# Optimization experiments

Measured on AMD Instinct MI355X. Metric: run time of the kernel, lower is better.

Reference implementation:

```python
import jax, jax.numpy as jnp
import numpy as np

B, U, V = 4, 64, 256
IN_DIM, STATE_DIM, CODE_DIM = 768, 768, 384
NUM_HEADS, HEAD_DIM = 8, 64
INNER = NUM_HEADS * HEAD_DIM  # 512
SCALE = HEAD_DIM ** 0.5


def _ln(x, g, b, eps=1e-5):
    mu = jnp.mean(x, axis=-1, keepdims=True)
    var = jnp.var(x, axis=-1, keepdims=True)
    return (x - mu) * jax.lax.rsqrt(var + eps) * g + b


def setup_inputs() -> dict:
    key = jax.random.key(0)
    ks = jax.random.split(key, 12)
    def w(k, shape, s=0.02):
        return jax.random.normal(k, shape, jnp.float32) * s
    return {
        "receiver_states": jax.random.normal(ks[0], (B, U, STATE_DIM), jnp.float32),
        "receiver_codes": jax.random.normal(ks[1], (B, U, CODE_DIM), jnp.float32),
        "sender_states": jax.random.normal(ks[2], (B, V, IN_DIM), jnp.float32),
        "ln_r_g": jnp.ones((STATE_DIM,), jnp.float32),
        "ln_r_b": jnp.zeros((STATE_DIM,), jnp.float32),
        "ln_s_g": jnp.ones((IN_DIM,), jnp.float32),
        "ln_s_b": jnp.zeros((IN_DIM,), jnp.float32),
        "Wq": w(ks[3], (STATE_DIM, INNER)), "bq": jnp.zeros((INNER,), jnp.float32), "Wmq": w(ks[4], (CODE_DIM, STATE_DIM)),
        "Wk": w(ks[5], (IN_DIM, INNER)),   "bk": jnp.zeros((INNER,), jnp.float32), "Wmk": w(ks[6], (CODE_DIM, IN_DIM)),
        "Wv": w(ks[7], (IN_DIM, INNER)),   "bv": jnp.zeros((INNER,), jnp.float32), "Wmv": w(ks[8], (CODE_DIM, IN_DIM)),
        "We": w(ks[9], (INNER, STATE_DIM)), "be": jnp.zeros((STATE_DIM,), jnp.float32), "Wme": w(ks[10], (CODE_DIM, INNER)),
        "gamma": jnp.ones((STATE_DIM,), jnp.float32),  # LayerScale, init 1.0
    }


def reference(receiver_states, receiver_codes, sender_states,
              ln_r_g, ln_r_b, ln_s_g, ln_s_b,
              Wq, bq, Wmq, Wk, bk, Wmk, Wv, bv, Wmv, We, be, Wme, gamma):
    r = _ln(receiver_states, ln_r_g, ln_r_b)   # (b,u,ds)
    s = _ln(sender_states, ln_s_g, ln_s_b)     # (b,v,di)
    # ModFC: y = (x * (1 + ctx @ Wm)) @ W + b  (code-conditioned input modulation)
    q = (r * (1.0 + receiver_codes @ Wmq)) @ Wq + bq          # (b,u,inner)
    mk = 1.0 + receiver_codes @ Wmk                           # (b,u,di)
    mv = 1.0 + receiver_codes @ Wmv                           # (b,u,di)
    xs = s[:, :, None, :]                                     # (b,v,1,di)
    k = (xs * mk[:, None, :, :]) @ Wk + bk                    # (b,v,u,inner)
    v = (xs * mv[:, None, :, :]) @ Wv + bv                    # (b,v,u,inner)
    qh = q.reshape(B, U, NUM_HEADS, HEAD_DIM)
    kh = k.reshape(B, V, U, NUM_HEADS, HEAD_DIM)
    vh = v.reshape(B, V, U, NUM_HEADS, HEAD_DIM)
    scores = jnp.einsum('buhc,bvuhc->bhuv', qh, kh) / SCALE   # (b,h,u,v)
    weights = jax.nn.softmax(scores, axis=-1)
    msg = jnp.einsum('bhuv,bvuhc->buhc', weights, vh).reshape(B, U, INNER)
    out = (msg * (1.0 + receiver_codes @ Wme)) @ We + be      # exit ModFC -> (b,u,ds)
    out = out * gamma                                         # LayerScale
    return receiver_states + out                              # residual
```

## Files before the change

### kernel.cpp

```cpp
#include <hip/hip_runtime.h>


#define DD 768
#define CDIM 384
#define NH 8
#define HD 64
#define INNER 512
#define VV 256

__device__ __forceinline__ void fma4(float4& a, float s, const float4& b) {
  a.x += s * b.x; a.y += s * b.y; a.z += s * b.z; a.w += s * b.w;
}

template <int K, int NS>
__device__ __forceinline__ void gcore(const float* __restrict__ A0, int lda,
                                      const float* __restrict__ Bp,
                                      float4& a0, float4& a1, float4& a2,
                                      float4& a3) {
  float4 b0[8], b1[8];
#pragma unroll
  for (int i = 0; i < 8; i++) b0[i] = *(const float4*)(Bp + (size_t)i * NS);
  const float* Bq = Bp + (size_t)8 * NS;
#pragma unroll 1
  for (int kk = 0; kk < K; kk += 16) {
#pragma unroll
    for (int i = 0; i < 8; i++) b1[i] = *(const float4*)(Bq + (size_t)i * NS);
    Bq += (size_t)8 * NS;
#pragma unroll
    for (int c = 0; c < 2; c++) {
      int kb = kk + c * 4;
      float4 f0 = *(const float4*)(A0 + kb);
      float4 f1 = *(const float4*)(A0 + lda + kb);
      float4 f2 = *(const float4*)(A0 + 2 * lda + kb);
      float4 f3 = *(const float4*)(A0 + 3 * lda + kb);
      float4 bv;
      bv = b0[c*4+0]; fma4(a0,f0.x,bv); fma4(a1,f1.x,bv); fma4(a2,f2.x,bv); fma4(a3,f3.x,bv);
      bv = b0[c*4+1]; fma4(a0,f0.y,bv); fma4(a1,f1.y,bv); fma4(a2,f2.y,bv); fma4(a3,f3.y,bv);
      bv = b0[c*4+2]; fma4(a0,f0.z,bv); fma4(a1,f1.z,bv); fma4(a2,f2.z,bv); fma4(a3,f3.z,bv);
      bv = b0[c*4+3]; fma4(a0,f0.w,bv); fma4(a1,f1.w,bv); fma4(a2,f2.w,bv); fma4(a3,f3.w,bv);
    }
    if (kk + 16 < K) {
#pragma unroll
      for (int i = 0; i < 8; i++) b0[i] = *(const float4*)(Bq + (size_t)i * NS);
      Bq += (size_t)8 * NS;
    }
#pragma unroll
    for (int c = 0; c < 2; c++) {
      int kb = kk + 8 + c * 4;
      float4 f0 = *(const float4*)(A0 + kb);
      float4 f1 = *(const float4*)(A0 + lda + kb);
      float4 f2 = *(const float4*)(A0 + 2 * lda + kb);
      float4 f3 = *(const float4*)(A0 + 3 * lda + kb);
      float4 bv;
      bv = b1[c*4+0]; fma4(a0,f0.x,bv); fma4(a1,f1.x,bv); fma4(a2,f2.x,bv); fma4(a3,f3.x,bv);
      bv = b1[c*4+1]; fma4(a0,f0.y,bv); fma4(a1,f1.y,bv); fma4(a2,f2.y,bv); fma4(a3,f3.y,bv);
      bv = b1[c*4+2]; fma4(a0,f0.z,bv); fma4(a1,f1.z,bv); fma4(a2,f2.z,bv); fma4(a3,f3.z,bv);
      bv = b1[c*4+3]; fma4(a0,f0.w,bv); fma4(a1,f1.w,bv); fma4(a2,f2.w,bv); fma4(a3,f3.w,bv);
    }
  }
}

__global__ __launch_bounds__(256, 2) void k_s1(
    const float* __restrict__ ss, const float* __restrict__ rs,
    const float* __restrict__ g_s, const float* __restrict__ b_s,
    const float* __restrict__ g_r, const float* __restrict__ b_r,
    const float* __restrict__ codes, const float* __restrict__ Wmq,
    const float* __restrict__ Wmk, const float* __restrict__ Wmv,
    const float* __restrict__ Wme, const float* __restrict__ Wk,
    const float* __restrict__ be, const float* __restrict__ gamma,
    float* __restrict__ s_ln, float* __restrict__ r_ln,
    float* __restrict__ cp, float* __restrict__ WkT,
    float* __restrict__ outp) {
  __shared__ __align__(16) float SB[6400];
  int bid = blockIdx.x, t = threadIdx.x;
  if (bid < 176) {
    int nc = bid % 11, mb = bid / 11;
    int base = nc * 256;
    const float* W; int N, colW;
    if (base < 768)       { W = Wmq; N = DD;    colW = base; }
    else if (base < 1536) { W = Wmk; N = DD;    colW = base - 768; }
    else if (base < 2304) { W = Wmv; N = DD;    colW = base - 1536; }
    else                  { W = Wme; N = INNER; colW = base - 2304; }
    int m0 = mb * 16;
#pragma unroll
    for (int p = 0; p < 24; p++) {
      int idx = p * 256 + t, r = idx / 384, k = idx % 384;
      SB[idx] = codes[(size_t)(m0 + r) * CDIM + k];
    }
    __syncthreads();
    int kl = t & 63, wid = t >> 6;
    const float* A0 = SB + (wid * 4) * 384;
    float4 a0 = {0,0,0,0}, a1 = {0,0,0,0}, a2 = {0,0,0,0}, a3 = {0,0,0,0};
    if (N == DD)
      gcore<384, DD>(A0, 384, W + colW + 4 * kl, a0, a1, a2, a3);
    else
      gcore<384, INNER>(A0, 384, W + colW + 4 * kl, a0, a1, a2, a3);
    int m = m0 + wid * 4, gcol = base + 4 * kl;
    *(float4*)(cp + (size_t)m * 2816 + gcol) = a0;
    *(float4*)(cp + (size_t)(m + 1) * 2816 + gcol) = a1;
    *(float4*)(cp + (size_t)(m + 2) * 2816 + gcol) = a2;
    *(float4*)(cp + (size_t)(m + 3) * 2816 + gcol) = a3;
  } else if (bid < 272) {
    int tid = bid - 176;
    int d0 = (tid >> 3) * 64, c0 = (tid & 7) * 64;
    int j = t & 63, i0 = t >> 6;
#pragma unroll
    for (int p = 0; p < 16; p++) {
      int i = p * 4 + i0;
      SB[i * 65 + j] = Wk[(size_t)(d0 + i) * INNER + c0 + j];
    }
    __syncthreads();
#pragma unroll
    for (int p = 0; p < 16; p++) {
      int i = p * 4 + i0;
      WkT[(size_t)(c0 + i) * DD + d0 + j] = SB[j * 65 + i];
    }
  } else {
    int rr = bid - 272;
    const float *x, *g, *bb; float* y; int r; bool isR;
    if (rr < 1024) { x = ss; g = g_s; bb = b_s; y = s_ln; r = rr; isR = false; }
    else           { x = rs; g = g_r; bb = b_r; y = r_ln; r = rr - 1024; isR = true; }
    const float* xr = x + (size_t)r * DD;
    float v0 = xr[t], v1 = xr[t + 256], v2 = xr[t + 512];
    float s = v0 + v1 + v2, sq = v0 * v0 + v1 * v1 + v2 * v2;
    for (int o = 32; o > 0; o >>= 1) {
      s += __shfl_down(s, o, 64); sq += __shfl_down(sq, o, 64);
    }
    int wid = t >> 6, lane = t & 63;
    if (lane == 0) { SB[wid] = s; SB[wid + 4] = sq; }
    __syncthreads();
    float sum = SB[0] + SB[1] + SB[2] + SB[3];
    float ssq = SB[4] + SB[5] + SB[6] + SB[7];
    float mu = sum * (1.0f / 768.0f);
    float var = ssq * (1.0f / 768.0f) - mu * mu;
    float rstd = rsqrtf(var + 1e-5f);
    float* yr = y + (size_t)r * DD;
    yr[t]       = (v0 - mu) * rstd * g[t]       + bb[t];
    yr[t + 256] = (v1 - mu) * rstd * g[t + 256] + bb[t + 256];
    yr[t + 512] = (v2 - mu) * rstd * g[t + 512] + bb[t + 512];
    if (isR) {
      float* orow = outp + (size_t)r * DD;
      orow[t]       = v0 + be[t]       * gamma[t];
      orow[t + 256] = v1 + be[t + 256] * gamma[t + 256];
      orow[t + 512] = v2 + be[t + 512] * gamma[t + 512];
    }
  }
}

__global__ __launch_bounds__(256, 2) void k_s2(
    const float* __restrict__ s_ln, const float* __restrict__ r_ln,
    const float* __restrict__ cp, const float* __restrict__ Wq,
    float* __restrict__ sT, float* __restrict__ qp) {
  __shared__ __align__(16) float SB[4160];
  int bid = blockIdx.x, t = threadIdx.x;
  if (bid < 128) {
    int ks = bid & 3, t2 = bid >> 2, nc = t2 & 1, mb = t2 >> 1;
    int m0 = mb * 16, col0 = nc * 256, k0 = ks * 192;
#pragma unroll
    for (int p = 0; p < 12; p++) {
      int idx = p * 256 + t, r = idx / 192, k = idx % 192;
      int d = k0 + k;
      float mqv = cp[(size_t)(m0 + r) * 2816 + d] + 1.0f;
      SB[idx] = r_ln[(size_t)(m0 + r) * DD + d] * mqv;
    }
    __syncthreads();
    int kl = t & 63, wid = t >> 6;
    int col = col0 + 4 * kl;
    const float* A0 = SB + (wid * 4) * 192;
    float4 a0 = {0,0,0,0}, a1 = {0,0,0,0}, a2 = {0,0,0,0}, a3 = {0,0,0,0};
    gcore<192, INNER>(A0, 192, Wq + (size_t)k0 * INNER + col, a0, a1, a2, a3);
    int m = m0 + wid * 4;
    float* dst = qp + (size_t)ks * (256 * INNER);
    *(float4*)(dst + (size_t)m * INNER + col) = a0;
    *(float4*)(dst + (size_t)(m + 1) * INNER + col) = a1;
    *(float4*)(dst + (size_t)(m + 2) * INNER + col) = a2;
    *(float4*)(dst + (size_t)(m + 3) * INNER + col) = a3;
  } else {
    int tid = bid - 128;
    int vt = tid & 3, dt = (tid >> 2) % 12, b = tid / 48;
    int v0 = vt * 64, d0 = dt * 64;
    int j = t & 63, i0 = t >> 6;
#pragma unroll
    for (int p = 0; p < 16; p++) {
      int i = p * 4 + i0;
      SB[i * 65 + j] = s_ln[(size_t)(b * VV + v0 + i) * DD + d0 + j];
    }
    __syncthreads();
#pragma unroll
    for (int p = 0; p < 16; p++) {
      int i = p * 4 + i0;
      sT[((size_t)b * DD + d0 + i) * VV + v0 + j] = SB[j * 65 + i];
    }
  }
}

__global__ __launch_bounds__(256, 2) void k_s3(
    const float* __restrict__ qp, const float* __restrict__ bq,
    const float* __restrict__ WkT, const float* __restrict__ cp,
    const float* __restrict__ bk, float* __restrict__ qm,
    float* __restrict__ qbk) {
  __shared__ __align__(16) float SB[1024];
  int bid = blockIdx.x, t = threadIdx.x;
  if (bid < 384) {
    int h = bid & 7, dc = (bid >> 3) % 3, mb = bid / 24;
    int m0 = mb * 16;
#pragma unroll
    for (int p = 0; p < 4; p++) {
      int idx = p * 256 + t, r = idx >> 6, c = idx & 63;
      int i = h * HD + c;
      size_t off = (size_t)(m0 + r) * INNER + i;
      SB[idx] = qp[off] + qp[131072 + off] + qp[262144 + off] +
                qp[393216 + off] + bq[i];
    }
    __syncthreads();
    int kl = t & 63, wid = t >> 6;
    int col = dc * 256 + 4 * kl;
    const float* A0 = SB + (wid * 4) * HD;
    float4 a0 = {0,0,0,0}, a1 = {0,0,0,0}, a2 = {0,0,0,0}, a3 = {0,0,0,0};
    gcore<64, DD>(A0, HD, WkT + (size_t)(h * HD) * DD + col, a0, a1, a2, a3);
#pragma unroll
    for (int j = 0; j < 4; j++) {
      float4 a = (j == 0) ? a0 : (j == 1) ? a1 : (j == 2) ? a2 : a3;
      int m = m0 + wid * 4 + j;
      const float* mkp = cp + (size_t)m * 2816 + 768 + col;
      float4 o = {a.x * (mkp[0] + 1.0f), a.y * (mkp[1] + 1.0f),
                  a.z * (mkp[2] + 1.0f), a.w * (mkp[3] + 1.0f)};
      *(float4*)(qm + ((size_t)m * NH + h) * DD + col) = o;
    }
  } else {
    int m = bid - 384;
    size_t off = (size_t)m * INNER;
    SB[t] = (qp[off + t] + qp[131072 + off + t] + qp[262144 + off + t] +
             qp[393216 + off + t] + bq[t]) * bk[t];
    int t2 = t + 256;
    SB[t2] = (qp[off + t2] + qp[131072 + off + t2] + qp[262144 + off + t2] +
              qp[393216 + off + t2] + bq[t2]) * bk[t2];
    __syncthreads();
    if (t < 8) {
      float a = 0.f;
      for (int c = 0; c < HD; c++) a += SB[t * HD + c];
      qbk[m * NH + t] = a;
    }
  }
}

__global__ __launch_bounds__(256, 2) void k_s4(
    const float* __restrict__ qm, const float* __restrict__ sT,
    float* __restrict__ scp) {
  __shared__ __align__(16) float SB[3072];
  int bid = blockIdx.x, t = threadIdx.x;
  int ks = bid & 3, b = (bid >> 2) & 3, mb = bid >> 4;
  int gi0 = b * 512 + mb * 16, k0 = ks * 192;
#pragma unroll
  for (int p = 0; p < 12; p++) {
    int idx = p * 256 + t, r = idx / 192, k = idx % 192;
    SB[idx] = qm[(size_t)(gi0 + r) * DD + k0 + k];
  }
  __syncthreads();
  int kl = t & 63, wid = t >> 6;
  int col = 4 * kl;
  const float* A0 = SB + (wid * 4) * 192;
  float4 a0 = {0,0,0,0}, a1 = {0,0,0,0}, a2 = {0,0,0,0}, a3 = {0,0,0,0};
  gcore<192, VV>(A0, 192, sT + ((size_t)b * DD + k0) * VV + col, a0, a1, a2, a3);
  int gi = gi0 + wid * 4;
  float* dst = scp + (size_t)ks * (2048 * VV);
  *(float4*)(dst + (size_t)gi * VV + col) = a0;
  *(float4*)(dst + (size_t)(gi + 1) * VV + col) = a1;
  *(float4*)(dst + (size_t)(gi + 2) * VV + col) = a2;
  *(float4*)(dst + (size_t)(gi + 3) * VV + col) = a3;
}

__global__ __launch_bounds__(256, 2) void k_s5(
    const float* __restrict__ scp, const float* __restrict__ qbk,
    const float* __restrict__ s_ln, const float* __restrict__ cp,
    float* __restrict__ wsm) {
  __shared__ __align__(16) float SB[4096];
  int bid = blockIdx.x, t = threadIdx.x;
  int dc = bid % 3, up = (bid / 3) % 32, b = bid / 96;
  int gi0 = b * 512 + up * 16;
#pragma unroll
  for (int p = 0; p < 16; p++) {
    int idx = p * 256 + t, r = idx >> 8, c = idx & 255;
    size_t o = (size_t)(gi0 + r) * VV + c;
    float v = scp[o] + scp[524288 + o] + scp[1048576 + o] + scp[1572864 + o];
    int m = b * 64 + up * 2 + (r >> 3), h = r & 7;
    SB[idx] = (v + qbk[m * NH + h]) * 0.125f;
  }
  __syncthreads();
  int wid = t >> 6, lane = t & 63;
#pragma unroll
  for (int j = 0; j < 4; j++) {
    int r = wid * 4 + j;
    float x0 = SB[r * 256 + lane],       x1 = SB[r * 256 + lane + 64];
    float x2 = SB[r * 256 + lane + 128], x3 = SB[r * 256 + lane + 192];
    float mx = fmaxf(fmaxf(x0, x1), fmaxf(x2, x3));
    for (int o = 1; o < 64; o <<= 1) mx = fmaxf(mx, __shfl_xor(mx, o, 64));
    float e0 = __expf(x0 - mx), e1 = __expf(x1 - mx);
    float e2 = __expf(x2 - mx), e3 = __expf(x3 - mx);
    float sm = e0 + e1 + e2 + e3;
    for (int o = 1; o < 64; o <<= 1) sm += __shfl_xor(sm, o, 64);
    float rinv = 1.0f / sm;
    SB[r * 256 + lane] = e0 * rinv;       SB[r * 256 + lane + 64] = e1 * rinv;
    SB[r * 256 + lane + 128] = e2 * rinv; SB[r * 256 + lane + 192] = e3 * rinv;
  }
  __syncthreads();
  int kl = t & 63;
  int col = dc * 256 + 4 * kl;
  const float* A0 = SB + (wid * 4) * 256;
  float4 a0 = {0,0,0,0}, a1 = {0,0,0,0}, a2 = {0,0,0,0}, a3 = {0,0,0,0};
  gcore<VV, DD>(A0, 256, s_ln + (size_t)(b * VV) * DD + col, a0, a1, a2, a3);
#pragma unroll
  for (int j = 0; j < 4; j++) {
    float4 a = (j == 0) ? a0 : (j == 1) ? a1 : (j == 2) ? a2 : a3;
    int r = wid * 4 + j;
    int ul = r >> 3, h = r & 7, m = b * 64 + up * 2 + ul;
    const float* mvp = cp + (size_t)m * 2816 + 1536 + col;
    float4 o = {a.x * (mvp[0] + 1.0f), a.y * (mvp[1] + 1.0f),
                a.z * (mvp[2] + 1.0f), a.w * (mvp[3] + 1.0f)};
    *(float4*)(wsm + ((size_t)h * 256 + m) * DD + col) = o;
  }
}

__global__ __launch_bounds__(256, 2) void k_s6(
    const float* __restrict__ wsm, const float* __restrict__ Wv,
    float* __restrict__ mmp) {
  __shared__ __align__(16) float SB[6400];
  int bid = blockIdx.x, t = threadIdx.x;
  int hp = bid & 1, ks = (bid >> 1) & 7, mb = bid >> 4;
  int h0 = hp * 4, m0 = mb * 16, k0 = ks * 96;
#pragma unroll
  for (int p = 0; p < 24; p++) {
    int idx = p * 256 + t;
    int e = idx / 1536, rem = idx % 1536, r = rem / 96, k = rem % 96;
    SB[e * 1540 + r * 96 + k] =
        wsm[((size_t)(h0 + e) * 256 + m0 + r) * DD + k0 + k];
  }
  __syncthreads();
  int kl = t & 63, wid = t >> 6;
  int hs = kl >> 4, c4 = 4 * (kl & 15);
  int colg = h0 * HD + hs * HD + c4;
  const float* A0 = SB + hs * 1540 + (wid * 4) * 96;
  float4 a0 = {0,0,0,0}, a1 = {0,0,0,0}, a2 = {0,0,0,0}, a3 = {0,0,0,0};
  gcore<96, INNER>(A0, 96, Wv + (size_t)k0 * INNER + colg, a0, a1, a2, a3);
  float* dst = mmp + (size_t)ks * (256 * INNER);
  int m = m0 + wid * 4;
  *(float4*)(dst + (size_t)m * INNER + colg) = a0;
  *(float4*)(dst + (size_t)(m + 1) * INNER + colg) = a1;
  *(float4*)(dst + (size_t)(m + 2) * INNER + colg) = a2;
  *(float4*)(dst + (size_t)(m + 3) * INNER + colg) = a3;
}

__global__ __launch_bounds__(256, 2) void k_s7(
    const float* __restrict__ mmp, const float* __restrict__ bvv,
    const float* __restrict__ cp, const float* __restrict__ We,
    const float* __restrict__ gamma, float* __restrict__ outp) {
  __shared__ __align__(16) float SB[1024];
  int bid = blockIdx.x, t = threadIdx.x;
  int ks = bid & 7, dc = (bid >> 3) % 3, mb = bid / 24;
  int m0 = mb * 16, k0 = ks * 64;
#pragma unroll
  for (int p = 0; p < 4; p++) {
    int idx = p * 256 + t, r = idx >> 6, k = idx & 63;
    int i = k0 + k;
    size_t off = (size_t)(m0 + r) * INNER + i;
    float v = mmp[off] + mmp[131072 + off] + mmp[262144 + off] +
              mmp[393216 + off] + mmp[524288 + off] + mmp[655360 + off] +
              mmp[786432 + off] + mmp[917504 + off];
    float mev = cp[(size_t)(m0 + r) * 2816 + 2304 + i] + 1.0f;
    SB[idx] = (v + bvv[i]) * mev;
  }
  __syncthreads();
  int kl = t & 63, wid = t >> 6;
  int col = dc * 256 + 4 * kl;
  const float* A0 = SB + (wid * 4) * 64;
  float4 a0 = {0,0,0,0}, a1 = {0,0,0,0}, a2 = {0,0,0,0}, a3 = {0,0,0,0};
  gcore<64, DD>(A0, 64, We + (size_t)k0 * DD + col, a0, a1, a2, a3);
  float4 g4 = *(const float4*)(gamma + col);
  int m = m0 + wid * 4;
#pragma unroll
  for (int j = 0; j < 4; j++) {
    float4 a = (j == 0) ? a0 : (j == 1) ? a1 : (j == 2) ? a2 : a3;
    float* orow = outp + (size_t)(m + j) * DD + col;
    unsafeAtomicAdd(orow + 0, a.x * g4.x);
    unsafeAtomicAdd(orow + 1, a.y * g4.y);
    unsafeAtomicAdd(orow + 2, a.z * g4.z);
    unsafeAtomicAdd(orow + 3, a.w * g4.w);
  }
}

extern "C" void kernel_launch(void* const* d_in, const int* in_sizes, int n_in,
                              void* d_out, int out_size, void* d_ws, size_t ws_size,
                              hipStream_t stream) {
  const float* rs     = (const float*)d_in[0];
  const float* codes  = (const float*)d_in[1];
  const float* ss     = (const float*)d_in[2];
  const float* ln_r_g = (const float*)d_in[3];
  const float* ln_r_b = (const float*)d_in[4];
  const float* ln_s_g = (const float*)d_in[5];
  const float* ln_s_b = (const float*)d_in[6];
  const float* Wq  = (const float*)d_in[7];
  const float* bq  = (const float*)d_in[8];
  const float* Wmq = (const float*)d_in[9];
  const float* Wk  = (const float*)d_in[10];
  const float* bk  = (const float*)d_in[11];
  const float* Wmk = (const float*)d_in[12];
  const float* Wv  = (const float*)d_in[13];
  const float* bv  = (const float*)d_in[14];
  const float* Wmv = (const float*)d_in[15];
  const float* We  = (const float*)d_in[16];
  const float* be  = (const float*)d_in[17];
  const float* Wme = (const float*)d_in[18];
  const float* gamma = (const float*)d_in[19];

  float* w = (float*)d_ws;
  float* s_ln = w;
  float* r_ln = w + 786432;
  float* WkT  = w + 983040;
  float* qp   = w + 1376256;
  float* sT   = w + 1900544;
  float* cp   = w + 2686976;
  float* qbk  = w + 3407872;
  float* qm   = w + 3409920;
  float* scp  = w + 4982784;
  float* wsm  = qm;
  float* mmp  = r_ln;

  k_s1<<<dim3(1552), 256, 0, stream>>>(ss, rs, ln_s_g, ln_s_b, ln_r_g, ln_r_b,
                                       codes, Wmq, Wmk, Wmv, Wme, Wk, be, gamma,
                                       s_ln, r_ln, cp, WkT, (float*)d_out);
  k_s2<<<dim3(320), 256, 0, stream>>>(s_ln, r_ln, cp, Wq, sT, qp);
  k_s3<<<dim3(640), 256, 0, stream>>>(qp, bq, WkT, cp, bk, qm, qbk);
  k_s4<<<dim3(512), 256, 0, stream>>>(qm, sT, scp);
  k_s5<<<dim3(384), 256, 0, stream>>>(scp, qbk, s_ln, cp, wsm);
  k_s6<<<dim3(256), 256, 0, stream>>>(wsm, Wv, mmp);
  k_s7<<<dim3(384), 256, 0, stream>>>(mmp, bv, cp, We, gamma, (float*)d_out);
}
```

Baseline: 213.3 us.

## Convert weights to bf16 in a prepass and replace output atomics with split-K reduction kernel

A new prepass kernel converts all eight weight matrices to bf16 each call, writing Wk transposed, and every GEMM core now reads bf16 weights and expands them to fp32 in registers. The goal is to halve weight memory traffic in the FMA-based GEMMs. Separately, the exit projection now writes per-split partial sums to a workspace, and a new final kernel reduces them and applies residual, bias and gamma, replacing float atomics. In exchange it adds two launches and a full conversion pass every call, and bf16 weights reduce accuracy.

```diff
diff --git a/kernel.cpp b/kernel.cpp
--- a/kernel.cpp
+++ b/kernel.cpp
@@ -8,8 +8,23 @@
 #define INNER 512
 #define VV 256
 
+typedef unsigned short u16;
+
 __device__ __forceinline__ void fma4(float4& a, float s, const float4& b) {
   a.x += s * b.x; a.y += s * b.y; a.z += s * b.z; a.w += s * b.w;
+}
+
+__device__ __forceinline__ float4 bexp(uint2 u) {
+  float4 r;
+  r.x = __uint_as_float(u.x << 16);
+  r.y = __uint_as_float(u.x & 0xffff0000u);
+  r.z = __uint_as_float(u.y << 16);
+  r.w = __uint_as_float(u.y & 0xffff0000u);
+  return r;
+}
+
+__device__ __forceinline__ u16 f2b(float v) {
+  return (u16)((__float_as_uint(v) + 0x8000u) >> 16);
 }
 
 template <int K, int NS>
@@ -60,27 +75,113 @@
   }
 }
 
+template <int K, int NS>
+__device__ __forceinline__ void gcoreb(const float* __restrict__ A0, int lda,
+                                       const u16* __restrict__ Bp,
+                                       float4& a0, float4& a1, float4& a2,
+                                       float4& a3) {
+  uint2 b0[8], b1[8];
+#pragma unroll
+  for (int i = 0; i < 8; i++) b0[i] = *(const uint2*)(Bp + (size_t)i * NS);
+  const u16* Bq = Bp + (size_t)8 * NS;
+#pragma unroll 1
+  for (int kk = 0; kk < K; kk += 16) {
+#pragma unroll
+    for (int i = 0; i < 8; i++) b1[i] = *(const uint2*)(Bq + (size_t)i * NS);
+    Bq += (size_t)8 * NS;
+#pragma unroll
+    for (int c = 0; c < 2; c++) {
+      int kb = kk + c * 4;
+      float4 f0 = *(const float4*)(A0 + kb);
+      float4 f1 = *(const float4*)(A0 + lda + kb);
+      float4 f2 = *(const float4*)(A0 + 2 * lda + kb);
+      float4 f3 = *(const float4*)(A0 + 3 * lda + kb);
+      float4 bv;
+      bv = bexp(b0[c*4+0]); fma4(a0,f0.x,bv); fma4(a1,f1.x,bv); fma4(a2,f2.x,bv); fma4(a3,f3.x,bv);
+      bv = bexp(b0[c*4+1]); fma4(a0,f0.y,bv); fma4(a1,f1.y,bv); fma4(a2,f2.y,bv); fma4(a3,f3.y,bv);
+      bv = bexp(b0[c*4+2]); fma4(a0,f0.z,bv); fma4(a1,f1.z,bv); fma4(a2,f2.z,bv); fma4(a3,f3.z,bv);
+      bv = bexp(b0[c*4+3]); fma4(a0,f0.w,bv); fma4(a1,f1.w,bv); fma4(a2,f2.w,bv); fma4(a3,f3.w,bv);
+    }
+    if (kk + 16 < K) {
+#pragma unroll
+      for (int i = 0; i < 8; i++) b0[i] = *(const uint2*)(Bq + (size_t)i * NS);
+      Bq += (size_t)8 * NS;
+    }
+#pragma unroll
+    for (int c = 0; c < 2; c++) {
+      int kb = kk + 8 + c * 4;
+      float4 f0 = *(const float4*)(A0 + kb);
+      float4 f1 = *(const float4*)(A0 + lda + kb);
+      float4 f2 = *(const float4*)(A0 + 2 * lda + kb);
+      float4 f3 = *(const float4*)(A0 + 3 * lda + kb);
+      float4 bv;
+      bv = bexp(b1[c*4+0]); fma4(a0,f0.x,bv); fma4(a1,f1.x,bv); fma4(a2,f2.x,bv); fma4(a3,f3.x,bv);
+      bv = bexp(b1[c*4+1]); fma4(a0,f0.y,bv); fma4(a1,f1.y,bv); fma4(a2,f2.y,bv); fma4(a3,f3.y,bv);
+      bv = bexp(b1[c*4+2]); fma4(a0,f0.z,bv); fma4(a1,f1.z,bv); fma4(a2,f2.z,bv); fma4(a3,f3.z,bv);
+      bv = bexp(b1[c*4+3]); fma4(a0,f0.w,bv); fma4(a1,f1.w,bv); fma4(a2,f2.w,bv); fma4(a3,f3.w,bv);
+    }
+  }
+}
+
+
+__global__ __launch_bounds__(256) void k_s0(
+    const float* __restrict__ Wmq, const float* __restrict__ Wmk,
+    const float* __restrict__ Wmv, const float* __restrict__ Wme,
+    const float* __restrict__ Wq, const float* __restrict__ Wk,
+    const float* __restrict__ Wv, const float* __restrict__ We,
+    u16* __restrict__ bw) {
+  __shared__ float TL[64 * 65];
+  int bid = blockIdx.x, t = threadIdx.x;
+  if (bid < 96) {
+    int d0 = (bid >> 3) * 64, c0 = (bid & 7) * 64;
+    int j = t & 63, i0 = t >> 6;
+#pragma unroll
+    for (int p = 0; p < 16; p++) {
+      int i = p * 4 + i0;
+      TL[i * 65 + j] = Wk[(size_t)(d0 + i) * INNER + c0 + j];
+    }
+    __syncthreads();
+    u16* dst = bw + 2260992;
+#pragma unroll
+    for (int p = 0; p < 16; p++) {
+      int i = p * 4 + i0;
+      dst[(size_t)(c0 + i) * DD + d0 + j] = f2b(TL[j * 65 + i]);
+    }
+  } else {
+    for (int idx = (bid - 96) * 256 + t; idx < 565248; idx += 1184 * 256) {
+      const float* src; u16* dst; int off;
+      if (idx < 73728)       { src = Wmq; dst = bw;           off = idx; }
+      else if (idx < 147456) { src = Wmk; dst = bw + 294912;  off = idx - 73728; }
+      else if (idx < 221184) { src = Wmv; dst = bw + 589824;  off = idx - 147456; }
+      else if (idx < 270336) { src = Wme; dst = bw + 884736;  off = idx - 221184; }
+      else if (idx < 368640) { src = Wq;  dst = bw + 1081344; off = idx - 270336; }
+      else if (idx < 466944) { src = Wv;  dst = bw + 1474560; off = idx - 368640; }
+      else                   { src = We;  dst = bw + 1867776; off = idx - 466944; }
+      float4 v = *(const float4*)(src + (size_t)off * 4);
+      ushort4 o;
+      o.x = f2b(v.x); o.y = f2b(v.y); o.z = f2b(v.z); o.w = f2b(v.w);
+      *(ushort4*)(dst + (size_t)off * 4) = o;
+    }
+  }
+}
+
 __global__ __launch_bounds__(256, 2) void k_s1(
     const float* __restrict__ ss, const float* __restrict__ rs,
     const float* __restrict__ g_s, const float* __restrict__ b_s,
     const float* __restrict__ g_r, const float* __restrict__ b_r,
-    const float* __restrict__ codes, const float* __restrict__ Wmq,
-    const float* __restrict__ Wmk, const float* __restrict__ Wmv,
-    const float* __restrict__ Wme, const float* __restrict__ Wk,
-    const float* __restrict__ be, const float* __restrict__ gamma,
+    const float* __restrict__ codes, const u16* __restrict__ bw,
     float* __restrict__ s_ln, float* __restrict__ r_ln,
-    float* __restrict__ cp, float* __restrict__ WkT,
-    float* __restrict__ outp) {
+    float* __restrict__ cp) {
   __shared__ __align__(16) float SB[6400];
   int bid = blockIdx.x, t = threadIdx.x;
   if (bid < 176) {
     int nc = bid % 11, mb = bid / 11;
     int base = nc * 256;
-    const float* W; int N, colW;
-    if (base < 768)       { W = Wmq; N = DD;    colW = base; }
-    else if (base < 1536) { W = Wmk; N = DD;    colW = base - 768; }
-    else if (base < 2304) { W = Wmv; N = DD;    colW = base - 1536; }
-    else                  { W = Wme; N = INNER; colW = base - 2304; }
+    const u16* W; int N, colW;
+    if (base < 768)       { W = bw;          N = DD;    colW = base; }
+    else if (base < 1536) { W = bw + 294912; N = DD;    colW = base - 768; }
+    else if (base < 2304) { W = bw + 589824; N = DD;    colW = base - 1536; }
+    else                  { W = bw + 884736; N = INNER; colW = base - 2304; }
     int m0 = mb * 16;
 #pragma unroll
     for (int p = 0; p < 24; p++) {
@@ -92,34 +193,19 @@
     const float* A0 = SB + (wid * 4) * 384;
     float4 a0 = {0,0,0,0}, a1 = {0,0,0,0}, a2 = {0,0,0,0}, a3 = {0,0,0,0};
     if (N == DD)
-      gcore<384, DD>(A0, 384, W + colW + 4 * kl, a0, a1, a2, a3);
+      gcoreb<384, DD>(A0, 384, W + colW + 4 * kl, a0, a1, a2, a3);
     else
-      gcore<384, INNER>(A0, 384, W + colW + 4 * kl, a0, a1, a2, a3);
+      gcoreb<384, INNER>(A0, 384, W + colW + 4 * kl, a0, a1, a2, a3);
     int m = m0 + wid * 4, gcol = base + 4 * kl;
     *(float4*)(cp + (size_t)m * 2816 + gcol) = a0;
     *(float4*)(cp + (size_t)(m + 1) * 2816 + gcol) = a1;
     *(float4*)(cp + (size_t)(m + 2) * 2816 + gcol) = a2;
     *(float4*)(cp + (size_t)(m + 3) * 2816 + gcol) = a3;
-  } else if (bid < 272) {
-    int tid = bid - 176;
-    int d0 = (tid >> 3) * 64, c0 = (tid & 7) * 64;
-    int j = t & 63, i0 = t >> 6;
-#pragma unroll
-    for (int p = 0; p < 16; p++) {
-      int i = p * 4 + i0;
-      SB[i * 65 + j] = Wk[(size_t)(d0 + i) * INNER + c0 + j];
-    }
-    __syncthreads();
-#pragma unroll
-    for (int p = 0; p < 16; p++) {
-      int i = p * 4 + i0;
-      WkT[(size_t)(c0 + i) * DD + d0 + j] = SB[j * 65 + i];
-    }
   } else {
-    int rr = bid - 272;
-    const float *x, *g, *bb; float* y; int r; bool isR;
-    if (rr < 1024) { x = ss; g = g_s; bb = b_s; y = s_ln; r = rr; isR = false; }
-    else           { x = rs; g = g_r; bb = b_r; y = r_ln; r = rr - 1024; isR = true; }
+    int rr = bid - 176;
+    const float *x, *g, *bb; float* y; int r;
+    if (rr < 1024) { x = ss; g = g_s; bb = b_s; y = s_ln; r = rr; }
+    else           { x = rs; g = g_r; bb = b_r; y = r_ln; r = rr - 1024; }
     const float* xr = x + (size_t)r * DD;
     float v0 = xr[t], v1 = xr[t + 256], v2 = xr[t + 512];
     float s = v0 + v1 + v2, sq = v0 * v0 + v1 * v1 + v2 * v2;
@@ -138,18 +224,12 @@
     yr[t]       = (v0 - mu) * rstd * g[t]       + bb[t];
     yr[t + 256] = (v1 - mu) * rstd * g[t + 256] + bb[t + 256];
     yr[t + 512] = (v2 - mu) * rstd * g[t + 512] + bb[t + 512];
-    if (isR) {
-      float* orow = outp + (size_t)r * DD;
-      orow[t]       = v0 + be[t]       * gamma[t];
-      orow[t + 256] = v1 + be[t + 256] * gamma[t + 256];
-      orow[t + 512] = v2 + be[t + 512] * gamma[t + 512];
-    }
   }
 }
 
 __global__ __launch_bounds__(256, 2) void k_s2(
     const float* __restrict__ s_ln, const float* __restrict__ r_ln,
-    const float* __restrict__ cp, const float* __restrict__ Wq,
+    const float* __restrict__ cp, const u16* __restrict__ bw,
     float* __restrict__ sT, float* __restrict__ qp) {
   __shared__ __align__(16) float SB[4160];
   int bid = blockIdx.x, t = threadIdx.x;
@@ -168,7 +248,8 @@
     int col = col0 + 4 * kl;
     const float* A0 = SB + (wid * 4) * 192;
     float4 a0 = {0,0,0,0}, a1 = {0,0,0,0}, a2 = {0,0,0,0}, a3 = {0,0,0,0};
-    gcore<192, INNER>(A0, 192, Wq + (size_t)k0 * INNER + col, a0, a1, a2, a3);
+    gcoreb<192, INNER>(A0, 192, bw + 1081344 + (size_t)k0 * INNER + col,
+                       a0, a1, a2, a3);
     int m = m0 + wid * 4;
     float* dst = qp + (size_t)ks * (256 * INNER);
     *(float4*)(dst + (size_t)m * INNER + col) = a0;
@@ -196,7 +277,7 @@
 
 __global__ __launch_bounds__(256, 2) void k_s3(
     const float* __restrict__ qp, const float* __restrict__ bq,
-    const float* __restrict__ WkT, const float* __restrict__ cp,
+    const u16* __restrict__ bw, const float* __restrict__ cp,
     const float* __restrict__ bk, float* __restrict__ qm,
     float* __restrict__ qbk) {
   __shared__ __align__(16) float SB[1024];
@@ -217,7 +298,8 @@
     int col = dc * 256 + 4 * kl;
     const float* A0 = SB + (wid * 4) * HD;
     float4 a0 = {0,0,0,0}, a1 = {0,0,0,0}, a2 = {0,0,0,0}, a3 = {0,0,0,0};
-    gcore<64, DD>(A0, HD, WkT + (size_t)(h * HD) * DD + col, a0, a1, a2, a3);
+    gcoreb<64, DD>(A0, HD, bw + 2260992 + (size_t)(h * HD) * DD + col,
+                   a0, a1, a2, a3);
 #pragma unroll
     for (int j = 0; j < 4; j++) {
       float4 a = (j == 0) ? a0 : (j == 1) ? a1 : (j == 2) ? a2 : a3;
@@ -322,7 +404,7 @@
 }
 
 __global__ __launch_bounds__(256, 2) void k_s6(
-    const float* __restrict__ wsm, const float* __restrict__ Wv,
+    const float* __restrict__ wsm, const u16* __restrict__ bw,
     float* __restrict__ mmp) {
   __shared__ __align__(16) float SB[6400];
   int bid = blockIdx.x, t = threadIdx.x;
@@ -341,7 +423,8 @@
   int colg = h0 * HD + hs * HD + c4;
   const float* A0 = SB + hs * 1540 + (wid * 4) * 96;
   float4 a0 = {0,0,0,0}, a1 = {0,0,0,0}, a2 = {0,0,0,0}, a3 = {0,0,0,0};
-  gcore<96, INNER>(A0, 96, Wv + (size_t)k0 * INNER + colg, a0, a1, a2, a3);
+  gcoreb<96, INNER>(A0, 96, bw + 1474560 + (size_t)k0 * INNER + colg,
+                    a0, a1, a2, a3);
   float* dst = mmp + (size_t)ks * (256 * INNER);
   int m = m0 + wid * 4;
   *(float4*)(dst + (size_t)m * INNER + colg) = a0;
@@ -352,8 +435,8 @@
 
 __global__ __launch_bounds__(256, 2) void k_s7(
     const float* __restrict__ mmp, const float* __restrict__ bvv,
-    const float* __restrict__ cp, const float* __restrict__ We,
-    const float* __restrict__ gamma, float* __restrict__ outp) {
+    const float* __restrict__ cp, const u16* __restrict__ bw,
+    float* __restrict__ op) {
   __shared__ __align__(16) float SB[1024];
   int bid = blockIdx.x, t = threadIdx.x;
   int ks = bid & 7, dc = (bid >> 3) % 3, mb = bid / 24;
@@ -374,17 +457,28 @@
   int col = dc * 256 + 4 * kl;
   const float* A0 = SB + (wid * 4) * 64;
   float4 a0 = {0,0,0,0}, a1 = {0,0,0,0}, a2 = {0,0,0,0}, a3 = {0,0,0,0};
-  gcore<64, DD>(A0, 64, We + (size_t)k0 * DD + col, a0, a1, a2, a3);
-  float4 g4 = *(const float4*)(gamma + col);
+  gcoreb<64, DD>(A0, 64, bw + 1867776 + (size_t)k0 * DD + col, a0, a1, a2, a3);
+  float* dst = op + (size_t)ks * (256 * DD);
   int m = m0 + wid * 4;
-#pragma unroll
-  for (int j = 0; j < 4; j++) {
-    float4 a = (j == 0) ? a0 : (j == 1) ? a1 : (j == 2) ? a2 : a3;
-    float* orow = outp + (size_t)(m + j) * DD + col;
-    unsafeAtomicAdd(orow + 0, a.x * g4.x);
-    unsafeAtomicAdd(orow + 1, a.y * g4.y);
-    unsafeAtomicAdd(orow + 2, a.z * g4.z);
-    unsafeAtomicAdd(orow + 3, a.w * g4.w);
+  *(float4*)(dst + (size_t)m * DD + col) = a0;
+  *(float4*)(dst + (size_t)(m + 1) * DD + col) = a1;
+  *(float4*)(dst + (size_t)(m + 2) * DD + col) = a2;
+  *(float4*)(dst + (size_t)(m + 3) * DD + col) = a3;
+}
+
+__global__ __launch_bounds__(256) void k_s8(
+    const float* __restrict__ op, const float* __restrict__ be,
+    const float* __restrict__ gamma, const float* __restrict__ rs,
+    float* __restrict__ outp) {
+  int m = blockIdx.x, t = threadIdx.x;
+#pragma unroll
+  for (int j = 0; j < 3; j++) {
+    int d = t + j * 256;
+    size_t off = (size_t)m * DD + d;
+    float v = op[off] + op[196608 + off] + op[393216 + off] +
+              op[589824 + off] + op[786432 + off] + op[983040 + off] +
+              op[1179648 + off] + op[1376256 + off];
+    outp[off] = rs[off] + (v + be[d]) * gamma[d];
   }
 }
 
@@ -415,7 +509,6 @@
   float* w = (float*)d_ws;
   float* s_ln = w;
   float* r_ln = w + 786432;
-  float* WkT  = w + 983040;
   float* qp   = w + 1376256;
   float* sT   = w + 1900544;
   float* cp   = w + 2686976;
@@ -424,14 +517,17 @@
   float* scp  = w + 4982784;
   float* wsm  = qm;
   float* mmp  = r_ln;
-
-  k_s1<<<dim3(1552), 256, 0, stream>>>(ss, rs, ln_s_g, ln_s_b, ln_r_g, ln_r_b,
-                                       codes, Wmq, Wmk, Wmv, Wme, Wk, be, gamma,
-                                       s_ln, r_ln, cp, WkT, (float*)d_out);
-  k_s2<<<dim3(320), 256, 0, stream>>>(s_ln, r_ln, cp, Wq, sT, qp);
-  k_s3<<<dim3(640), 256, 0, stream>>>(qp, bq, WkT, cp, bk, qm, qbk);
+  float* op   = scp;
+  u16*   bw   = (u16*)(w + 7079936);
+
+  k_s0<<<dim3(1280), 256, 0, stream>>>(Wmq, Wmk, Wmv, Wme, Wq, Wk, Wv, We, bw);
+  k_s1<<<dim3(1456), 256, 0, stream>>>(ss, rs, ln_s_g, ln_s_b, ln_r_g, ln_r_b,
+                                       codes, bw, s_ln, r_ln, cp);
+  k_s2<<<dim3(320), 256, 0, stream>>>(s_ln, r_ln, cp, bw, sT, qp);
+  k_s3<<<dim3(640), 256, 0, stream>>>(qp, bq, bw, cp, bk, qm, qbk);
   k_s4<<<dim3(512), 256, 0, stream>>>(qm, sT, scp);
   k_s5<<<dim3(384), 256, 0, stream>>>(scp, qbk, s_ln, cp, wsm);
-  k_s6<<<dim3(256), 256, 0, stream>>>(wsm, Wv, mmp);
-  k_s7<<<dim3(384), 256, 0, stream>>>(mmp, bv, cp, We, gamma, (float*)d_out);
-}
+  k_s6<<<dim3(256), 256, 0, stream>>>(wsm, bw, mmp);
+  k_s7<<<dim3(384), 256, 0, stream>>>(mmp, bv, cp, bw, op);
+  k_s8<<<dim3(256), 256, 0, stream>>>(op, be, gamma, rs, (float*)d_out);
+}
```

After: 204.7 us. 1.04x faster.
